# Kernel tuning notes

Hardware: AMD Instinct MI355X
Metric: run time of the kernel (lower is better)

## Reference

```python
import jax, jax.numpy as jnp
import numpy as np


def setup_inputs() -> dict:
    key = jax.random.key(0)
    k1, k2, k3, k4 = jax.random.split(key, 4)
    N, T, F = 8192, 128, 9
    M_s = 256
    merged = jax.random.normal(k1, (N, T, F), dtype=jnp.float32)
    input1 = jax.random.normal(k2, (N, T, F), dtype=jnp.float32)
    samples = jax.random.normal(k3, (N, M_s), dtype=jnp.float32)
    labels = jax.random.randint(k4, (N,), 0, 10, dtype=jnp.int32)
    return {"merged": merged, "input1": input1, "samples": samples, "labels": labels}


def reference(merged, input1, samples, labels):
    # Pairwise squared distances S_ij = sum_k (s_i - s_j)^2 / M_s, computed via
    # the Gram-matrix identity instead of materializing the [N, N, M_s] tensor.
    M_s = samples.shape[1]
    sq = jnp.sum(samples * samples, axis=-1)                 # [N]
    gram = jnp.einsum('im,jm->ij', samples, samples)         # [N, N]
    S_ij = (sq[:, None] + sq[None, :] - 2.0 * gram) / jnp.float32(M_s)
    same = (labels[:, None] == labels[None, :]).astype(jnp.float32)
    term2 = jnp.mean(jnp.maximum(0.0, (1.0 - same) * (1.0 - S_ij)))
    L_label = 10.0 * jnp.mean(same * S_ij) + 10.0 * term2
    return L_label
```

## Files before the change

### kernel.cpp

```cpp
#include <hip/hip_runtime.h>

#define NROWS 8192
#define KDIM  256
#define NT    64
#define NBLK  (NT * (NT + 1) / 2)
#define GRID  256

typedef __attribute__((ext_vector_type(4)))  float f32x4;
typedef __attribute__((ext_vector_type(16))) float f32x16;
typedef __attribute__((ext_vector_type(4)))  int   i32x4;
typedef __attribute__((ext_vector_type(8)))  int   i32x8;

#define GLD(gp, lp)                                                            \
  __builtin_amdgcn_global_load_lds(                                            \
      (const __attribute__((address_space(1))) void*)(gp),                     \
      (__attribute__((address_space(3))) void*)(lp), 16, 0, 0)

__global__ __launch_bounds__(256) void prep_kernel(
    const float* __restrict__ samples, const int* __restrict__ labels,
    unsigned char* __restrict__ sf8, float2* __restrict__ meta,
    float* __restrict__ out) {
  int tid = blockIdx.x * 256 + threadIdx.x;
  int gw = tid >> 6;
  int lane = tid & 63;
#pragma unroll
  for (int it = 0; it < NROWS / 1024; ++it) {
    int row = gw + it * 1024;
    f32x4 v = ((const f32x4*)samples)[(size_t)row * 64 + lane];
    int pk = __builtin_amdgcn_cvt_pk_fp8_f32(v.x, v.y, 0, false);
    pk = __builtin_amdgcn_cvt_pk_fp8_f32(v.z, v.w, pk, true);
    ((unsigned int*)sf8)[(size_t)row * 64 + lane] = (unsigned int)pk;
    float p = v.x * v.x + v.y * v.y + v.z * v.z + v.w * v.w;
#pragma unroll
    for (int off = 32; off; off >>= 1) p += __shfl_down(p, off);
    if (lane == 0)
      meta[row] = make_float2(p * (1.0f / 256.0f), (float)labels[row]);
  }
  if (tid == 0) out[0] = 0.0f;
}

__device__ inline void decode_tile(int b, int& bi, int& bj) {
  float disc = (2.0f * NT + 1.0f) * (2.0f * NT + 1.0f) - 8.0f * (float)b;
  bi = (int)(((2.0f * NT + 1.0f) - sqrtf(disc)) * 0.5f);
  if (bi < 0) bi = 0;
  if (bi > NT - 1) bi = NT - 1;
  while (bi > 0 && (bi * NT - bi * (bi - 1) / 2) > b) --bi;
  while (((bi + 1) * NT - (bi + 1) * bi / 2) <= b) ++bi;
  bj = bi + (b - (bi * NT - bi * (bi - 1) / 2));
}

__global__ __launch_bounds__(512, 1) void pair_kernel(
    const unsigned char* __restrict__ sf8, const float2* __restrict__ meta,
    float* __restrict__ out) {

  __shared__ __align__(16) unsigned char As[2][128 * 256];
  __shared__ __align__(16) unsigned char Bs[2][128 * 256];
  __shared__ float red[8];

  int t = threadIdx.x;
  int lane = t & 63;
  int w = t >> 6;
  int wm = w >> 1, wn = w & 1;
  int lr = lane >> 4, pc = lane & 15;
  int l31 = lane & 31;
  int hk  = lane >> 5;

  float stt = 0.f;

  auto stage_A = [&](int bi_, int buf) {
    int rA = bi_ * 128;
#pragma unroll
    for (int p = 0; p < 4; ++p) {
      int region = p * 8 + w;
      int rr = region * 4 + lr;
      int c = pc ^ (rr & 15);
      GLD(sf8 + (size_t)(rA + rr) * KDIM + c * 16, &As[buf][region * 1024]);
    }
  };
  auto stage_B = [&](int bj_, int buf) {
    int rB = bj_ * 128;
#pragma unroll
    for (int p = 0; p < 4; ++p) {
      int region = p * 8 + w;
      int rr = region * 4 + lr;
      int c = pc ^ (rr & 15);
      GLD(sf8 + (size_t)(rB + rr) * KDIM + c * 16, &Bs[buf][region * 1024]);
    }
  };

  int cid = (blockIdx.x & 7) * 32 + (blockIdx.x >> 3);
  int t0 = (cid * 65) >> 3, t1 = ((cid + 1) * 65) >> 3;
  int ntile = t1 - t0;

  int bi, bj;
  decode_tile(t0, bi, bj);
  stage_A(bi, 0);
  stage_B(bj, 0);
  int acur = 0, bcur = 0;

  int pbi = 0, pbj = 0;
  float sqa[16], laa[16], sqb[2], labv[2], pwt = 1.f;
  f32x16 accA[2], accB[2];

  auto load_scalars = [&](int pbi_, int pbj_) {
#pragma unroll
    for (int g = 0; g < 4; ++g) {
      int gr = pbi_ * 128 + wm * 32 + g * 8 + 4 * hk;
      f32x4 m0 = *(const f32x4*)(meta + gr);
      f32x4 m1 = *(const f32x4*)(meta + gr + 2);
      sqa[g * 4 + 0] = m0.x; laa[g * 4 + 0] = m0.y;
      sqa[g * 4 + 1] = m0.z; laa[g * 4 + 1] = m0.w;
      sqa[g * 4 + 2] = m1.x; laa[g * 4 + 2] = m1.y;
      sqa[g * 4 + 3] = m1.z; laa[g * 4 + 3] = m1.w;
    }
#pragma unroll
    for (int j = 0; j < 2; ++j) {
      float2 mb = meta[pbj_ * 128 + wn * 64 + j * 32 + l31];
      sqb[j] = mb.x; labv[j] = mb.y;
    }
    pwt = (pbi_ == pbj_) ? 1.0f : 2.0f;
  };

  auto domfma = [&](f32x16 (&acc)[2]) {
#pragma unroll
    for (int j = 0; j < 2; ++j)
#pragma unroll
      for (int e = 0; e < 16; ++e) acc[j][e] = 0.f;
    const unsigned char* Ab = &As[acur][0];
    const unsigned char* Bb = &Bs[bcur][0];
#pragma unroll
    for (int kt = 0; kt < 4; ++kt) {
      int c0 = kt * 4 + hk * 2;
      int m = wm * 32 + l31;
      const unsigned char* ab = Ab + m * 256;
      int sm = m & 15;
      i32x4 alo = *(const i32x4*)(ab + ((c0 ^ sm) << 4));
      i32x4 ahi = *(const i32x4*)(ab + (((c0 + 1) ^ sm) << 4));
      i32x8 av = {alo.x, alo.y, alo.z, alo.w, ahi.x, ahi.y, ahi.z, ahi.w};
#pragma unroll
      for (int j = 0; j < 2; ++j) {
        int n = wn * 64 + j * 32 + l31;
        const unsigned char* bb = Bb + n * 256;
        int sn = n & 15;
        i32x4 blo = *(const i32x4*)(bb + ((c0 ^ sn) << 4));
        i32x4 bhi = *(const i32x4*)(bb + (((c0 + 1) ^ sn) << 4));
        i32x8 bv = {blo.x, blo.y, blo.z, blo.w, bhi.x, bhi.y, bhi.z, bhi.w};
        acc[j] = __builtin_amdgcn_mfma_scale_f32_32x32x64_f8f6f4(
            av, bv, acc[j], 0, 0, 0, 127, 0, 127);
      }
    }
  };

  auto epi = [&](const f32x16 (&acc)[2]) {
    float s = 0.f;
#pragma unroll
    for (int j = 0; j < 2; ++j) {
#pragma unroll
      for (int g2 = 0; g2 < 16; ++g2) {
        float S = sqa[g2] + sqb[j] - acc[j][g2] * (1.0f / 128.0f);
        float h = fmaxf(0.f, 1.f - S);
        s += (laa[g2] == labv[j]) ? S : h;
      }
    }
    stt += pwt * s;
  };

  for (int k = 0; k < ntile; ++k) {
    bool have_next = (k + 1 < ntile);
    int nbi = bi, nbj = bj + 1;
    if (nbj == NT) { nbi = bi + 1; nbj = nbi; }

    __syncthreads();

    if (k > 0) load_scalars(pbi, pbj);

    if (have_next) {
      stage_B(nbj, bcur ^ 1);
      if (nbi != bi) stage_A(nbi, acur ^ 1);
    }

    if (k & 1) {
      domfma(accB);
      if (k > 0) epi(accA);
    } else {
      domfma(accA);
      if (k > 0) epi(accB);
    }

    pbi = bi; pbj = bj;
    if (have_next) {
      if (nbi != bi) acur ^= 1;
      bcur ^= 1;
      bi = nbi; bj = nbj;
    }
  }

  load_scalars(pbi, pbj);
  if ((ntile - 1) & 1) epi(accB);
  else                 epi(accA);

#pragma unroll
  for (int off = 32; off; off >>= 1) stt += __shfl_down(stt, off);
  if (lane == 0) red[w] = stt;
  __syncthreads();
  if (t == 0) {
    float a = 0.f;
#pragma unroll
    for (int q = 0; q < 8; q++) a += red[q];
    atomicAdd(&out[0], a * (10.0f / ((float)NROWS * (float)NROWS)));
  }
}

extern "C" void kernel_launch(void* const* d_in, const int* in_sizes, int n_in,
                              void* d_out, int out_size, void* d_ws,
                              size_t ws_size, hipStream_t stream) {
  const float* samples = (const float*)d_in[2];
  const int*   labels  = (const int*)d_in[3];

  char* ws = (char*)d_ws;
  unsigned char* sf8 = (unsigned char*)ws;
  float2* meta = (float2*)(ws + (size_t)NROWS * KDIM);
  float* out   = (float*)d_out;

  prep_kernel<<<GRID, 256, 0, stream>>>(samples, labels, sf8, meta, out);
  pair_kernel<<<GRID, 512, 0, stream>>>(sf8, meta, out);
}
```

Measured before the change: 124.8 us.

## Replace double-buffered persistent tile loop with single-buffer two-blocks-per-CU grid-stride

Drops the software-pipelined double buffering of the A/B fp8 tiles and the contiguous per-block tile ranges. Each block now stages one A and one B tile into single LDS buffers, syncs, computes and runs the epilogue in turn. Halving LDS use allows two 512-thread blocks per CU, with a grid of 512 walking triangle tiles in grid stride. The aim is to hide load latency through occupancy instead of in-block overlap. In exchange every tile reloads its A tile, there is no prefetch within a block, and the tail tiles are unbalanced (2080 tiles over 512 blocks).

```diff
diff --git a/kernel.cpp b/kernel.cpp
--- a/kernel.cpp
+++ b/kernel.cpp
@@ -4,7 +4,7 @@
 #define KDIM  256
 #define NT    64
 #define NBLK  (NT * (NT + 1) / 2)
-#define GRID  256
+#define GRID  512
 
 typedef __attribute__((ext_vector_type(4)))  float f32x4;
 typedef __attribute__((ext_vector_type(16))) float f32x16;
@@ -49,12 +49,12 @@
   bj = bi + (b - (bi * NT - bi * (bi - 1) / 2));
 }
 
-__global__ __launch_bounds__(512, 1) void pair_kernel(
+__global__ __launch_bounds__(512, 2) void pair_kernel(
     const unsigned char* __restrict__ sf8, const float2* __restrict__ meta,
     float* __restrict__ out) {
 
-  __shared__ __align__(16) unsigned char As[2][128 * 256];
-  __shared__ __align__(16) unsigned char Bs[2][128 * 256];
+  __shared__ __align__(16) unsigned char As[128 * 256];
+  __shared__ __align__(16) unsigned char Bs[128 * 256];
   __shared__ float red[8];
 
   int t = threadIdx.x;
@@ -67,45 +67,30 @@
 
   float stt = 0.f;
 
-  auto stage_A = [&](int bi_, int buf) {
-    int rA = bi_ * 128;
+  auto stage = [&](int bi_, int bj_) {
+    int rA = bi_ * 128, rB = bj_ * 128;
 #pragma unroll
     for (int p = 0; p < 4; ++p) {
       int region = p * 8 + w;
       int rr = region * 4 + lr;
       int c = pc ^ (rr & 15);
-      GLD(sf8 + (size_t)(rA + rr) * KDIM + c * 16, &As[buf][region * 1024]);
-    }
-  };
-  auto stage_B = [&](int bj_, int buf) {
-    int rB = bj_ * 128;
-#pragma unroll
-    for (int p = 0; p < 4; ++p) {
-      int region = p * 8 + w;
-      int rr = region * 4 + lr;
-      int c = pc ^ (rr & 15);
-      GLD(sf8 + (size_t)(rB + rr) * KDIM + c * 16, &Bs[buf][region * 1024]);
+      GLD(sf8 + (size_t)(rA + rr) * KDIM + c * 16, &As[region * 1024]);
+      GLD(sf8 + (size_t)(rB + rr) * KDIM + c * 16, &Bs[region * 1024]);
     }
   };
 
-  int cid = (blockIdx.x & 7) * 32 + (blockIdx.x >> 3);
-  int t0 = (cid * 65) >> 3, t1 = ((cid + 1) * 65) >> 3;
-  int ntile = t1 - t0;
+  int tile = blockIdx.x;
+  int bi, bj;
 
-  int bi, bj;
-  decode_tile(t0, bi, bj);
-  stage_A(bi, 0);
-  stage_B(bj, 0);
-  int acur = 0, bcur = 0;
+  while (tile < NBLK) {
+    decode_tile(tile, bi, bj);
 
-  int pbi = 0, pbj = 0;
-  float sqa[16], laa[16], sqb[2], labv[2], pwt = 1.f;
-  f32x16 accA[2], accB[2];
+    stage(bi, bj);
 
-  auto load_scalars = [&](int pbi_, int pbj_) {
+    float sqa[16], laa[16], sqb[2], labv[2];
 #pragma unroll
     for (int g = 0; g < 4; ++g) {
-      int gr = pbi_ * 128 + wm * 32 + g * 8 + 4 * hk;
+      int gr = bi * 128 + wm * 32 + g * 8 + 4 * hk;
       f32x4 m0 = *(const f32x4*)(meta + gr);
       f32x4 m1 = *(const f32x4*)(meta + gr + 2);
       sqa[g * 4 + 0] = m0.x; laa[g * 4 + 0] = m0.y;
@@ -115,32 +100,32 @@
     }
 #pragma unroll
     for (int j = 0; j < 2; ++j) {
-      float2 mb = meta[pbj_ * 128 + wn * 64 + j * 32 + l31];
+      float2 mb = meta[bj * 128 + wn * 64 + j * 32 + l31];
       sqb[j] = mb.x; labv[j] = mb.y;
     }
-    pwt = (pbi_ == pbj_) ? 1.0f : 2.0f;
-  };
+    float wt = (bi == bj) ? 1.0f : 2.0f;
 
-  auto domfma = [&](f32x16 (&acc)[2]) {
+    __syncthreads();
+
+    f32x16 acc[2];
 #pragma unroll
     for (int j = 0; j < 2; ++j)
 #pragma unroll
       for (int e = 0; e < 16; ++e) acc[j][e] = 0.f;
-    const unsigned char* Ab = &As[acur][0];
-    const unsigned char* Bb = &Bs[bcur][0];
+
+    int m = wm * 32 + l31;
+    const unsigned char* ab = &As[m * 256];
+    int sm = m & 15;
 #pragma unroll
     for (int kt = 0; kt < 4; ++kt) {
       int c0 = kt * 4 + hk * 2;
-      int m = wm * 32 + l31;
-      const unsigned char* ab = Ab + m * 256;
-      int sm = m & 15;
       i32x4 alo = *(const i32x4*)(ab + ((c0 ^ sm) << 4));
       i32x4 ahi = *(const i32x4*)(ab + (((c0 + 1) ^ sm) << 4));
       i32x8 av = {alo.x, alo.y, alo.z, alo.w, ahi.x, ahi.y, ahi.z, ahi.w};
 #pragma unroll
       for (int j = 0; j < 2; ++j) {
         int n = wn * 64 + j * 32 + l31;
-        const unsigned char* bb = Bb + n * 256;
+        const unsigned char* bb = &Bs[n * 256];
         int sn = n & 15;
         i32x4 blo = *(const i32x4*)(bb + ((c0 ^ sn) << 4));
         i32x4 bhi = *(const i32x4*)(bb + (((c0 + 1) ^ sn) << 4));
@@ -149,9 +134,7 @@
             av, bv, acc[j], 0, 0, 0, 127, 0, 127);
       }
     }
-  };
 
-  auto epi = [&](const f32x16 (&acc)[2]) {
     float s = 0.f;
 #pragma unroll
     for (int j = 0; j < 2; ++j) {
@@ -162,42 +145,11 @@
         s += (laa[g2] == labv[j]) ? S : h;
       }
     }
-    stt += pwt * s;
-  };
+    stt += wt * s;
 
-  for (int k = 0; k < ntile; ++k) {
-    bool have_next = (k + 1 < ntile);
-    int nbi = bi, nbj = bj + 1;
-    if (nbj == NT) { nbi = bi + 1; nbj = nbi; }
-
-    __syncthreads();
-
-    if (k > 0) load_scalars(pbi, pbj);
-
-    if (have_next) {
-      stage_B(nbj, bcur ^ 1);
-      if (nbi != bi) stage_A(nbi, acur ^ 1);
-    }
-
-    if (k & 1) {
-      domfma(accB);
-      if (k > 0) epi(accA);
-    } else {
-      domfma(accA);
-      if (k > 0) epi(accB);
-    }
-
-    pbi = bi; pbj = bj;
-    if (have_next) {
-      if (nbi != bi) acur ^= 1;
-      bcur ^= 1;
-      bi = nbi; bj = nbj;
-    }
+    tile += GRID;
+    if (tile < NBLK) __syncthreads();
   }
-
-  load_scalars(pbi, pbj);
-  if ((ntile - 1) & 1) epi(accB);
-  else                 epi(accA);
 
 #pragma unroll
   for (int off = 32; off; off >>= 1) stt += __shfl_down(stt, off);
@@ -222,6 +174,6 @@
   float2* meta = (float2*)(ws + (size_t)NROWS * KDIM);
   float* out   = (float*)d_out;
 
-  prep_kernel<<<GRID, 256, 0, stream>>>(samples, labels, sf8, meta, out);
+  prep_kernel<<<256, 256, 0, stream>>>(samples, labels, sf8, meta, out);
   pair_kernel<<<GRID, 512, 0, stream>>>(sf8, meta, out);
 }
```

Result: slower. 129.1 us (+3.5%).
